# Kernel optimization log

Measured on AMD Instinct MI355X. Metric: run time of the kernel, lower is better.

## Reference

```python
import jax, jax.numpy as jnp
import numpy as np

B, S, E, H = 4, 4096, 768, 8
D = E // H  # head_dim = 96


def setup_inputs() -> dict:
    key = jax.random.key(0)
    ks = jax.random.split(key, 9)
    std = 1.0 / np.sqrt(E)
    return {
        "values": jax.random.normal(ks[0], (B, S, E), dtype=jnp.float32),
        "keys": jax.random.normal(ks[1], (B, S, E), dtype=jnp.float32),
        "query": jax.random.normal(ks[2], (B, S, E), dtype=jnp.float32),
        "mask": jax.random.randint(ks[3], (B, S, 1, 1), 0, 2, dtype=jnp.int32),
        "Wv": jax.random.normal(ks[4], (E, E), dtype=jnp.float32) * std,
        "Wk": jax.random.normal(ks[5], (E, E), dtype=jnp.float32) * std,
        "Wq": jax.random.normal(ks[6], (E, E), dtype=jnp.float32) * std,
        "Wo": jax.random.normal(ks[7], (E, E), dtype=jnp.float32) * std,
        "bo": jax.random.normal(ks[8], (E,), dtype=jnp.float32) * std,
    }


def reference(values, keys, query, mask, Wv, Wk, Wq, Wo, bo):
    b, s, e = query.shape
    h, d = H, e // H
    scale = e ** 0.5

    def split(x, W):
        # Linear (no bias) then view to [b, s, h, d] and permute to [b, h, s, d]
        return (x @ W.T).reshape(b, s, h, d).transpose(0, 2, 1, 3)

    v = split(values, Wv)   # [b, h, s, d]
    k = split(keys, Wk)     # [b, h, s, d]
    q = split(query, Wq)    # [b, h, s, d]

    # Faithful to torch.einsum('nqhd,nkhd->nhqk', q, k) with q,k laid out as
    # [b, h, s, d]: this contracts over d with s batched, producing a per-token
    # head-gram matrix att[b, s, i, j] = sum_d q[b,i,s,d] * k[b,j,s,d].
    att = jnp.einsum('bisd,bjsd->bsij', q, k)          # [b, s, h, h]
    att = jnp.where(mask == 0, jnp.float32(-1e20), att)
    att = jax.nn.softmax(att / scale, axis=3)

    # torch.einsum('nhql,nlhd->nqhd', att, v) with att [b,s,h,h], v [b,h,s,d]:
    # out[b, i, s, d] = sum_j att[b,s,i,j] * v[b,j,s,d]  -> [b, h, s, d]
    out = jnp.einsum('bsij,bjsd->bisd', att, v)        # [b, h, s, d]
    out = out.reshape(b, s, h * d)                      # row-major, matches torch .reshape
    return out @ Wo.T + bo
```

## Files before the change

### kernel.cpp

```cpp
#include <hip/hip_runtime.h>
#include <hip/hip_bf16.h>
#include <cstdint>


typedef unsigned short u16;
typedef short bf16x8 __attribute__((ext_vector_type(8)));
typedef float f32x4 __attribute__((ext_vector_type(4)));

#define B_  4
#define S_  4096
#define E_  768
#define H_  8
#define D_  96
#define T_  (B_*S_)
#define BM_ 128
#define BN_ 128
#define NT_ (E_/BN_)

static __device__ __forceinline__ u16 f2bf(float f) {
  unsigned u = __builtin_bit_cast(unsigned, f);
  u += 0x7fffu + ((u >> 16) & 1u);
  return (u16)(u >> 16);
}
static __device__ __forceinline__ unsigned pk2(float lo, float hi) {
  return (unsigned)f2bf(lo) | ((unsigned)f2bf(hi) << 16);
}
static __device__ __forceinline__ float bflo(unsigned u) {
  return __builtin_bit_cast(float, u << 16);
}
static __device__ __forceinline__ float bfhi(unsigned u) {
  return __builtin_bit_cast(float, u & 0xffff0000u);
}

__global__ __launch_bounds__(256) void conv_w(
    const float* __restrict__ w0, const float* __restrict__ w1,
    const float* __restrict__ w2, const float* __restrict__ w3,
    u16* __restrict__ dst)
{
  const int bpw = (E_ * E_ / 4) / 256;
  const int which = blockIdx.x / bpw;
  const float* src = which == 0 ? w0 : which == 1 ? w1 : which == 2 ? w2 : w3;
  const int i = (blockIdx.x - which * bpw) * 256 + threadIdx.x;
  const float4 v = ((const float4*)src)[i];
  uint2 w;
  w.x = pk2(v.x, v.y);
  w.y = pk2(v.z, v.w);
  ((uint2*)(dst + (size_t)which * E_ * E_))[i] = w;
}

__global__ __launch_bounds__(256) void conv3(
    const float* __restrict__ q, const float* __restrict__ k,
    const float* __restrict__ v, u16* __restrict__ xq,
    u16* __restrict__ xk, u16* __restrict__ xv)
{
  const int w = blockIdx.y;
  const float* src = w == 0 ? q : w == 1 ? k : v;
  u16* dst = w == 0 ? xq : w == 1 ? xk : xv;
  const int i = blockIdx.x * 256 + threadIdx.x;
  const float4 vv = ((const float4*)src)[i];
  uint2 o;
  o.x = pk2(vv.x, vv.y);
  o.y = pk2(vv.z, vv.w);
  ((uint2*)dst)[i] = o;
}


#define GLOAD(SRC, DST)                                                        \
  __builtin_amdgcn_global_load_lds(                                            \
      (const __attribute__((address_space(1))) void*)(SRC),                    \
      (__attribute__((address_space(3))) void*)(DST), 16, 0, 0)

#define STAGE(BUF, KT)                                                         \
  {                                                                            \
    _Pragma("unroll")                                                          \
    for (int c = 0; c < 2; ++c) {                                              \
      const int idx = (c << 8) + tid;                                          \
      const int r = idx >> 2, g = idx & 3;                                     \
      const int gs = g ^ ((r >> 1) & 3);                                       \
      GLOAD(A + (size_t)(tM + r) * E_ + (KT) + (gs << 3),                      \
            &lds[BUF][0][((c << 8) + (wave << 6)) << 3]);                      \
      GLOAD(Wt + (size_t)(tN + r) * E_ + (KT) + (gs << 3),                     \
            &lds[BUF][1][((c << 8) + (wave << 6)) << 3]);                      \
    }                                                                          \
  }

#define LOADFRAGS(BUF)                                                         \
  {                                                                            \
    _Pragma("unroll")                                                          \
    for (int m = 0; m < 4; ++m)                                                \
      a[m] = *(const bf16x8*)&lds[BUF][0][(((wr << 6) + (m << 4) + l15) << 5) + slotOff]; \
    _Pragma("unroll")                                                          \
    for (int n = 0; n < 4; ++n)                                                \
      b[n] = *(const bf16x8*)&lds[BUF][1][(((wc << 6) + (n << 4) + l15) << 5) + slotOff]; \
  }

#define DOMFMA()                                                               \
  {                                                                            \
    _Pragma("unroll")                                                          \
    for (int m = 0; m < 4; ++m)                                                \
      _Pragma("unroll")                                                        \
      for (int n = 0; n < 4; ++n)                                              \
        acc[m][n] = __builtin_amdgcn_mfma_f32_16x16x32_bf16(a[m], b[n], acc[m][n], 0, 0, 0); \
  }

template<bool BATCHED, bool OUT_F32, bool BIAS>
__global__ __launch_bounds__(256, 3) void gemm_nt(
    const u16* __restrict__ a0, const u16* __restrict__ a1,
    const u16* __restrict__ a2, const u16* __restrict__ Wall,
    const float* __restrict__ bias,
    void* __restrict__ c0, void* __restrict__ c1, void* __restrict__ c2)
{
  __shared__ u16 lds[2][2][4096];
  const u16* A;
  const u16* Wt;
  void* Cv;
  if constexpr (BATCHED) {
    const int q_ = blockIdx.y;
    A  = q_ == 0 ? a0 : q_ == 1 ? a1 : a2;
    Wt = Wall + (size_t)q_ * (E_ * E_);
    Cv = q_ == 0 ? c0 : q_ == 1 ? c1 : c2;
  } else {
    A = a0; Wt = Wall; Cv = c0;
  }

  {
    int sidx = blockIdx.x >> 8;
    if constexpr (BATCHED) sidx = (sidx + 3 * blockIdx.y) % 5;
#pragma unroll 1
    for (int z = 0; z < sidx; ++z) __builtin_amdgcn_s_sleep(3);
  }

  const int tid  = threadIdx.x;
  const int wave = tid >> 6;
  const int lane = tid & 63;
  const int wr = wave >> 1, wc = wave & 1;
  const int bid = blockIdx.x;
  const int wg  = (bid & 7) * 96 + (bid >> 3);
  const int mT  = wg / NT_;
  const int nT  = wg - mT * NT_;
  const int tM = mT * BM_, tN = nT * BN_;
  const int l15 = lane & 15, l4 = lane >> 4;
  const int slotOff = (l4 ^ ((l15 >> 1) & 3)) << 3;

  f32x4 acc[4][4] = {};

  STAGE(0, 0);
  __syncthreads();

  for (int i = 0; i < 12; ++i) {
    const int kt = i << 6;
    {
      bf16x8 a[4], b[4];
      LOADFRAGS(0);
      STAGE(1, kt + 32);
      DOMFMA();
    }
    __syncthreads();
    {
      bf16x8 a[4], b[4];
      LOADFRAGS(1);
      if (i < 11) STAGE(0, kt + 64);
      DOMFMA();
    }
    __syncthreads();
  }

  if constexpr (OUT_F32) {
#pragma unroll
    for (int m = 0; m < 4; ++m) {
#pragma unroll
      for (int n = 0; n < 4; ++n) {
        const int row = tM + (wr << 6) + (m << 4) + (l4 << 2);
        const int col = tN + (wc << 6) + (n << 4) + l15;
        const float badd = BIAS ? bias[col] : 0.f;
#pragma unroll
        for (int r = 0; r < 4; ++r)
          ((float*)Cv)[(size_t)(row + r) * E_ + col] = acc[m][n][r] + badd;
      }
    }
  } else {
    __syncthreads();
    u16* lC = (u16*)lds;
#pragma unroll
    for (int m = 0; m < 4; ++m)
#pragma unroll
      for (int n = 0; n < 4; ++n) {
        const int row = (wr << 6) + (m << 4) + (l4 << 2);
        const int col = (wc << 6) + (n << 4) + l15;
#pragma unroll
        for (int r = 0; r < 4; ++r)
          lC[(row + r) * BN_ + col] = f2bf(acc[m][n][r]);
      }
    __syncthreads();
#pragma unroll
    for (int p = 0; p < 8; ++p) {
      const int row = (p << 4) + (wave << 2) + l4;
      const bf16x8 v = *(const bf16x8*)&lC[row * BN_ + (l15 << 3)];
      *(bf16x8*)((u16*)Cv + (size_t)(tM + row) * E_ + tN + (l15 << 3)) = v;
    }
  }
}

__global__ __launch_bounds__(256) void attn_tok(
    const u16* __restrict__ Q, const u16* __restrict__ K,
    const u16* __restrict__ V, const int* __restrict__ mask,
    u16* __restrict__ O)
{
  __shared__ float pl[4][8][8];
  const int tid = threadIdx.x, wave = tid >> 6, lane = tid & 63;
  const int t = blockIdx.x * 4 + wave;
  const int s = t & (S_ - 1);
  const int b = t >> 12;
  const int i = lane >> 3, j = lane & 7;

  const uint4* qp = (const uint4*)(Q + (size_t)t * E_ + i * D_);
  const uint4* kp = (const uint4*)(K + (size_t)t * E_ + j * D_);
  float acc = 0.f;
#pragma unroll
  for (int it = 0; it < 12; ++it) {
    const uint4 qv = qp[it], kv = kp[it];
    acc += bflo(qv.x) * bflo(kv.x) + bfhi(qv.x) * bfhi(kv.x);
    acc += bflo(qv.y) * bflo(kv.y) + bfhi(qv.y) * bfhi(kv.y);
    acc += bflo(qv.z) * bflo(kv.z) + bfhi(qv.z) * bfhi(kv.z);
    acc += bflo(qv.w) * bflo(kv.w) + bfhi(qv.w) * bfhi(kv.w);
  }
  float sv = (mask[t] == 0) ? -1e20f : acc;
  sv *= 0.03608439182435161f;
  float mx = sv;
  mx = fmaxf(mx, __shfl_xor(mx, 1));
  mx = fmaxf(mx, __shfl_xor(mx, 2));
  mx = fmaxf(mx, __shfl_xor(mx, 4));
  const float e = __expf(sv - mx);
  float sm = e;
  sm += __shfl_xor(sm, 1);
  sm += __shfl_xor(sm, 2);
  sm += __shfl_xor(sm, 4);
  pl[wave][i][j] = e / sm;
  __syncthreads();

  const int i2 = lane >> 3, db = lane & 7;
  float o[12] = {};
#pragma unroll
  for (int jj = 0; jj < 8; ++jj) {
    const float pj = pl[wave][i2][jj];
    const uint2* vp = (const uint2*)(V + (size_t)t * E_ + jj * D_ + db * 12);
    const uint2 v0 = vp[0], v1 = vp[1], v2 = vp[2];
    o[0]  += pj * bflo(v0.x);  o[1]  += pj * bfhi(v0.x);
    o[2]  += pj * bflo(v0.y);  o[3]  += pj * bfhi(v0.y);
    o[4]  += pj * bflo(v1.x);  o[5]  += pj * bfhi(v1.x);
    o[6]  += pj * bflo(v1.y);  o[7]  += pj * bfhi(v1.y);
    o[8]  += pj * bflo(v2.x);  o[9]  += pj * bfhi(v2.x);
    o[10] += pj * bflo(v2.y);  o[11] += pj * bfhi(v2.y);
  }
  const size_t row = (size_t)b * S_ + 512 * i2 + (s >> 3);
  u16* op = O + row * E_ + 96 * (s & 7) + db * 12;
  uint2 w0, w1, w2;
  w0.x = pk2(o[0], o[1]);
  w0.y = pk2(o[2], o[3]);
  w1.x = pk2(o[4], o[5]);
  w1.y = pk2(o[6], o[7]);
  w2.x = pk2(o[8], o[9]);
  w2.y = pk2(o[10], o[11]);
  ((uint2*)op)[0] = w0;
  ((uint2*)op)[1] = w1;
  ((uint2*)op)[2] = w2;
}

extern "C" void kernel_launch(void* const* d_in, const int* in_sizes, int n_in,
                              void* d_out, int out_size, void* d_ws, size_t ws_size,
                              hipStream_t stream)
{
  const float* values = (const float*)d_in[0];
  const float* keys   = (const float*)d_in[1];
  const float* query  = (const float*)d_in[2];
  const int*   mask   = (const int*)d_in[3];
  const float* Wv = (const float*)d_in[4];
  const float* Wk = (const float*)d_in[5];
  const float* Wq = (const float*)d_in[6];
  const float* Wo = (const float*)d_in[7];
  const float* bo = (const float*)d_in[8];

  const size_t TE = (size_t)T_ * E_;
  const size_t EE = (size_t)E_ * E_;
  u16* Qb = (u16*)d_ws;
  u16* Kb = Qb + TE;
  u16* Vb = Kb + TE;
  u16* Xq = Vb + TE;
  u16* Wb = Xq + TE;
  u16* Xk = (u16*)d_out;
  u16* Xv = Xk + TE;

  dim3 blk(256);

  conv_w<<<dim3(4 * (E_ * E_ / 4) / 256), blk, 0, stream>>>(Wq, Wk, Wv, Wo, Wb);

  conv3<<<dim3(TE / 4 / 256, 3), blk, 0, stream>>>(query, keys, values, Xq, Xk, Xv);

  gemm_nt<true, false, false><<<dim3(T_ / BM_ * NT_, 3), blk, 0, stream>>>(
      Xq, Xk, Xv, Wb, nullptr, Qb, Kb, Vb);

  attn_tok<<<dim3(T_ / 4), blk, 0, stream>>>(Qb, Kb, Vb, mask, Xq );

  gemm_nt<false, true, true><<<dim3(T_ / BM_ * NT_), blk, 0, stream>>>(
      Xq , nullptr, nullptr, Wb + 3 * EE, bo, (float*)d_out, nullptr, nullptr);
}
```

Before: 175.3 us.

## Triple-buffer LDS in GEMM and wait on partial vmcnt instead of full barrier

Moves the GEMM K-loop from two LDS stages to three, so global loads for the stage two steps ahead are in flight while the current stage is computed. The full __syncthreads is replaced by an inline s_waitcnt vmcnt(4) plus s_barrier, which waits only for the oldest stage's loads. The startup stagger is also changed to three groups. LDS use grows by half, which may limit blocks per CU, and the hand-written vmcnt counts depend on STAGE issuing exactly four vector loads per thread.

```diff
diff --git a/kernel.cpp b/kernel.cpp
--- a/kernel.cpp
+++ b/kernel.cpp
@@ -103,6 +103,15 @@
         acc[m][n] = __builtin_amdgcn_mfma_f32_16x16x32_bf16(a[m], b[n], acc[m][n], 0, 0, 0); \
   }
 
+#define STEP(RB, SB, KT, STG, VM)                                              \
+  {                                                                            \
+    bf16x8 a[4], b[4];                                                         \
+    LOADFRAGS(RB);                                                             \
+    if (STG) STAGE(SB, KT);                                                    \
+    DOMFMA();                                                                  \
+    asm volatile("s_waitcnt vmcnt(" #VM ")\n\ts_barrier" ::: "memory");        \
+  }
+
 template<bool BATCHED, bool OUT_F32, bool BIAS>
 __global__ __launch_bounds__(256, 3) void gemm_nt(
     const u16* __restrict__ a0, const u16* __restrict__ a1,
@@ -110,7 +119,7 @@
     const float* __restrict__ bias,
     void* __restrict__ c0, void* __restrict__ c1, void* __restrict__ c2)
 {
-  __shared__ u16 lds[2][2][4096];
+  __shared__ u16 lds[3][2][4096];
   const u16* A;
   const u16* Wt;
   void* Cv;
@@ -125,7 +134,7 @@
 
   {
     int sidx = blockIdx.x >> 8;
-    if constexpr (BATCHED) sidx = (sidx + 3 * blockIdx.y) % 5;
+    if constexpr (BATCHED) sidx = (sidx + blockIdx.y) % 3;
 #pragma unroll 1
     for (int z = 0; z < sidx; ++z) __builtin_amdgcn_s_sleep(3);
   }
@@ -145,24 +154,22 @@
   f32x4 acc[4][4] = {};
 
   STAGE(0, 0);
-  __syncthreads();
-
-  for (int i = 0; i < 12; ++i) {
-    const int kt = i << 6;
-    {
-      bf16x8 a[4], b[4];
-      LOADFRAGS(0);
-      STAGE(1, kt + 32);
-      DOMFMA();
-    }
-    __syncthreads();
-    {
-      bf16x8 a[4], b[4];
-      LOADFRAGS(1);
-      if (i < 11) STAGE(0, kt + 64);
-      DOMFMA();
-    }
-    __syncthreads();
+  STAGE(1, 32);
+  asm volatile("s_waitcnt vmcnt(4)\n\ts_barrier" ::: "memory");
+
+#pragma unroll 1
+  for (int it = 0; it < 7; ++it) {
+    const int kt = it * 96;
+    STEP(0, 2, kt + 64,  true, 4);
+    STEP(1, 0, kt + 96,  true, 4);
+    STEP(2, 1, kt + 128, true, 4);
+  }
+  STEP(0, 2, 736, true, 4);
+  STEP(1, 0, 0,   false, 0);
+  {
+    bf16x8 a[4], b[4];
+    LOADFRAGS(2);
+    DOMFMA();
   }
 
   if constexpr (OUT_F32) {
```

Result: faster. 169.0 us (-3.6%).
